# Performance work log

Measured on AMD Instinct MI355X. Metric: run time of the kernel, lower is better.

## Reference

```python
import jax, jax.numpy as jnp
import numpy as np


def _conv1x1(x, w, b):
    # x: [B,C,H,W], w: [O,C], b: [O] -> [B,O,H,W]
    return jnp.einsum('bchw,oc->bohw', x, w) + b[None, :, None, None]


def setup_inputs() -> dict:
    key = jax.random.key(0)
    ks = jax.random.split(key, 5)
    B, C, H, W = 4, 256, 64, 64
    C2 = C // 2
    scale = 0.02  # keep attention logits in a sane range
    return {
        'x': jax.random.normal(ks[0], (B, C, H, W), dtype=jnp.float32),
        'w_theta': jax.random.normal(ks[1], (C2, C), dtype=jnp.float32) * scale,
        'b_theta': jnp.zeros((C2,), dtype=jnp.float32),
        'w_phi': jax.random.normal(ks[2], (C2, C), dtype=jnp.float32) * scale,
        'b_phi': jnp.zeros((C2,), dtype=jnp.float32),
        'w_g': jax.random.normal(ks[3], (C2, C), dtype=jnp.float32) * scale,
        'b_g': jnp.zeros((C2,), dtype=jnp.float32),
        'w_out': jax.random.normal(ks[4], (C, C2), dtype=jnp.float32) * scale,
        'b_out': jnp.zeros((C,), dtype=jnp.float32),
    }


def reference(x, w_theta, b_theta, w_phi, b_phi, w_g, b_g, w_out, b_out):
    B, C, H, W = x.shape
    C2 = C // 2
    N = H * W
    theta = _conv1x1(x, w_theta, b_theta).reshape(B, C2, N)  # [B,C2,N]
    phi = _conv1x1(x, w_phi, b_phi).reshape(B, C2, N)        # [B,C2,N]
    g = _conv1x1(x, w_g, b_g).reshape(B, C2, N)              # [B,C2,N]
    # non-local attention: scores[b,m,n] = theta[b,:,m] . phi[b,:,n]
    scores = jnp.einsum('bcm,bcn->bmn', theta, phi)          # [B,N,N]
    attn = jax.nn.softmax(scores, axis=-1)                   # [B,N,N]
    # output = g @ attn^T : out[b,c,m] = sum_n g[b,c,n] * attn[b,m,n]
    out = jnp.einsum('bcn,bmn->bcm', g, attn)                # [B,C2,N]
    out = out.reshape(B, C2, H, W)
    return x + _conv1x1(out, w_out, b_out)
```

## Files before the change

### kernel.cpp

```cpp
#include <hip/hip_runtime.h>
#include <hip/hip_bf16.h>

#define B_  4
#define C_  256
#define C2_ 128
#define N_  4096
#define LOG2E 1.4426950408889634f

typedef unsigned short u16;
typedef __attribute__((ext_vector_type(8))) short bf16x8;
typedef __attribute__((ext_vector_type(4))) float f32x4;

static __device__ __forceinline__ u16 f2bf(float f) {
    return __builtin_bit_cast(u16, __float2bfloat16(f));
}
static __device__ __forceinline__ float bf2f(u16 u) {
    return __bfloat162float(__builtin_bit_cast(__hip_bfloat16, u));
}

__global__ __launch_bounds__(256) void prepw_kernel(
    const float* __restrict__ wt, const float* __restrict__ wp,
    const float* __restrict__ wg, const float* __restrict__ wo,
    u16* __restrict__ Wb) {
    int i = (blockIdx.x * 256 + threadIdx.x) * 4;
    int mat = i >> 15, off = i & 32767;
    const float* src = mat == 0 ? wt : (mat == 1 ? wp : (mat == 2 ? wg : wo));
    float4 v = *(const float4*)(src + off);
    ushort4 o = { f2bf(v.x), f2bf(v.y), f2bf(v.z), f2bf(v.w) };
    *(ushort4*)(Wb + i) = o;
}

__global__ __launch_bounds__(256) void projx_kernel(
    const float* __restrict__ x, const u16* __restrict__ Wb,
    const float* __restrict__ b_theta, const float* __restrict__ b_phi,
    const float* __restrict__ b_g,
    u16* __restrict__ Q, u16* __restrict__ K, u16* __restrict__ V) {
    __shared__ __align__(16) union {
        u16 XTs[32][264];
        u16 Vt[128][40];
    } sm;
    int bid = blockIdx.x;
    int b   = bid / (N_ / 32);
    int n0  = (bid % (N_ / 32)) * 32;
    int tid = threadIdx.x;
    int wave = tid >> 6, lane = tid & 63, quad = lane >> 4, l16 = lane & 15;
    int mgrp = wave >> 1, chalf = wave & 1;

#pragma unroll
    for (int it = 0; it < 4; ++it) {
        int idx = it * 256 + tid;
        int q = idx & 7, p = idx >> 3;
        const float* r0 = x + ((size_t)b * C_ + 2 * p) * N_ + n0 + 4 * q;
        float4 v0 = *(const float4*)r0;
        float4 v1 = *(const float4*)(r0 + N_);
        const float* f0 = (const float*)&v0;
        const float* f1 = (const float*)&v1;
#pragma unroll
        for (int j = 0; j < 4; ++j) {
            unsigned pk = (unsigned)f2bf(f0[j]) | ((unsigned)f2bf(f1[j]) << 16);
            *(unsigned*)&sm.XTs[4 * q + j][2 * p] = pk;
        }
    }
    __syncthreads();

    bf16x8 af[8];
#pragma unroll
    for (int ks = 0; ks < 8; ++ks)
        af[ks] = *(const bf16x8*)&sm.XTs[mgrp * 16 + l16][ks * 32 + quad * 8];
    __syncthreads();

    const float* biases[3] = { b_theta, b_phi, b_g };
#pragma unroll
    for (int mat = 0; mat < 3; ++mat) {
        const u16* wm = Wb + (size_t)mat * C2_ * C_;
        const float* bias = biases[mat];
        f32x4 acc[4];
#pragma unroll
        for (int i = 0; i < 4; ++i) acc[i] = (f32x4){0.f, 0.f, 0.f, 0.f};
#pragma unroll
        for (int ct = 0; ct < 4; ++ct) {
            int ce = chalf * 4 + ct;
            const u16* wr = wm + (size_t)(ce * 16 + l16) * C_ + quad * 8;
#pragma unroll
            for (int ks = 0; ks < 8; ++ks) {
                bf16x8 bf = *(const bf16x8*)(wr + ks * 32);
                acc[ct] = __builtin_amdgcn_mfma_f32_16x16x32_bf16(af[ks], bf, acc[ct], 0, 0, 0);
            }
        }
        if (mat < 2) {
            u16* dst = mat == 0 ? Q : K;
            float sc = mat == 0 ? LOG2E : 1.0f;
#pragma unroll
            for (int ct = 0; ct < 4; ++ct) {
                int c2 = (chalf * 4 + ct) * 16 + l16;
                float bb = bias[c2];
#pragma unroll
                for (int r = 0; r < 4; ++r) {
                    int n = n0 + mgrp * 16 + quad * 4 + r;
                    dst[((size_t)b * N_ + n) * C2_ + c2] = f2bf((acc[ct][r] + bb) * sc);
                }
            }
        } else {
#pragma unroll
            for (int ct = 0; ct < 4; ++ct) {
                int c2 = (chalf * 4 + ct) * 16 + l16;
                float bb = bias[c2];
#pragma unroll
                for (int r = 0; r < 4; ++r)
                    sm.Vt[c2][mgrp * 16 + quad * 4 + r] = f2bf(acc[ct][r] + bb);
            }
        }
    }
    __syncthreads();
    {
        int row = tid >> 1, col16 = (tid & 1) * 16;
        uint4 a0 = *(const uint4*)&sm.Vt[row][col16];
        uint4 a1 = *(const uint4*)&sm.Vt[row][col16 + 8];
        u16* vp = V + ((size_t)b * C2_ + row) * N_ + n0 + col16;
        *(uint4*)vp = a0;
        *(uint4*)(vp + 8) = a1;
    }
}

__global__ __launch_bounds__(256, 2) void attn_kernel(
    const u16* __restrict__ Q, const u16* __restrict__ K,
    const u16* __restrict__ V, u16* __restrict__ AO,
    u16* __restrict__ Opb, float* __restrict__ lsum, int nsplit) {
    const int BM = 128, BN = 64, D = C2_;
    const int per = B_ * (N_ / BM);
    int s    = blockIdx.x / per;
    int r0   = blockIdx.x % per;
    int b    = r0 / (N_ / BM);
    int m0   = (r0 % (N_ / BM)) * BM;
    int tid  = threadIdx.x;
    int wave = tid >> 6, lane = tid & 63, quad = (lane >> 4) & 3, l16 = lane & 15;

    __shared__ __align__(16) u16 Ks[BN][D + 8];
    __shared__ __align__(16) u16 Vs[D][BN + 8];
    __shared__ __align__(16) u16 Psb[4][32][BN + 8];
    u16* Ps = &Psb[wave][0][0];

    bf16x8 qf[2][4];
#pragma unroll
    for (int ms = 0; ms < 2; ++ms) {
        const u16* qp = Q + ((size_t)b * N_ + m0 + wave * 32 + ms * 16 + l16) * D;
#pragma unroll
        for (int kk = 0; kk < 4; ++kk)
            qf[ms][kk] = *(const bf16x8*)(qp + kk * 32 + quad * 8);
    }

    float l_r[2][4] = {{0.f, 0.f, 0.f, 0.f}, {0.f, 0.f, 0.f, 0.f}};
    f32x4 o_acc[2][8];
#pragma unroll
    for (int ms = 0; ms < 2; ++ms)
#pragma unroll
        for (int i = 0; i < 8; ++i) o_acc[ms][i] = (f32x4){0.f, 0.f, 0.f, 0.f};

    const int tiles = N_ / BN;
    const int base = tiles / nsplit, rem = tiles % nsplit;
    const int t0 = s * base + (s < rem ? s : rem);
    const int cnt = base + (s < rem ? 1 : 0);
    const int nt0 = t0 * BN, nt1 = (t0 + cnt) * BN;

    for (int nt = nt0; nt < nt1; nt += BN) {
        const u16* kp = K + ((size_t)b * N_ + nt) * D;
#pragma unroll
        for (int it = 0; it < 4; ++it) {
            int idx = it * 256 + tid;
            int row = idx >> 4, col = (idx & 15) * 8;
            *(uint4*)&Ks[row][col] = *(const uint4*)(kp + row * D + col);
        }
#pragma unroll
        for (int it = 0; it < 4; ++it) {
            int idx = it * 256 + tid;
            int row = idx >> 3, col = (idx & 7) * 8;
            *(uint4*)&Vs[row][col] =
                *(const uint4*)(V + ((size_t)b * C2_ + row) * N_ + nt + col);
        }
        __syncthreads();

        f32x4 sc[2][4];
#pragma unroll
        for (int nn = 0; nn < 4; ++nn) {
            f32x4 a0 = (f32x4){0.f, 0.f, 0.f, 0.f};
            f32x4 a1 = (f32x4){0.f, 0.f, 0.f, 0.f};
#pragma unroll
            for (int kk = 0; kk < 4; ++kk) {
                bf16x8 kf = *(const bf16x8*)&Ks[nn * 16 + l16][kk * 32 + quad * 8];
                a0 = __builtin_amdgcn_mfma_f32_16x16x32_bf16(qf[0][kk], kf, a0, 0, 0, 0);
                a1 = __builtin_amdgcn_mfma_f32_16x16x32_bf16(qf[1][kk], kf, a1, 0, 0, 0);
            }
            sc[0][nn] = a0;
            sc[1][nn] = a1;
        }

#pragma unroll
        for (int ms = 0; ms < 2; ++ms)
#pragma unroll
            for (int nn = 0; nn < 4; ++nn)
#pragma unroll
                for (int r = 0; r < 4; ++r) {
                    float p = __builtin_amdgcn_exp2f(sc[ms][nn][r]);
                    l_r[ms][r] += p;
                    Ps[(ms * 16 + quad * 4 + r) * (BN + 8) + nn * 16 + l16] = f2bf(p);
                }

#pragma unroll
        for (int ks = 0; ks < 2; ++ks) {
            bf16x8 pf0 = *(const bf16x8*)&Ps[(l16) * (BN + 8) + ks * 32 + quad * 8];
            bf16x8 pf1 = *(const bf16x8*)&Ps[(16 + l16) * (BN + 8) + ks * 32 + quad * 8];
#pragma unroll
            for (int cs = 0; cs < 8; ++cs) {
                bf16x8 vf = *(const bf16x8*)&Vs[cs * 16 + l16][ks * 32 + quad * 8];
                o_acc[0][cs] = __builtin_amdgcn_mfma_f32_16x16x32_bf16(pf0, vf, o_acc[0][cs], 0, 0, 0);
                o_acc[1][cs] = __builtin_amdgcn_mfma_f32_16x16x32_bf16(pf1, vf, o_acc[1][cs], 0, 0, 0);
            }
        }
        __syncthreads();
    }

#pragma unroll
    for (int ms = 0; ms < 2; ++ms)
#pragma unroll
        for (int r = 0; r < 4; ++r) {
            l_r[ms][r] += __shfl_xor(l_r[ms][r], 1);
            l_r[ms][r] += __shfl_xor(l_r[ms][r], 2);
            l_r[ms][r] += __shfl_xor(l_r[ms][r], 4);
            l_r[ms][r] += __shfl_xor(l_r[ms][r], 8);
        }

    if (Opb) {
#pragma unroll
        for (int ms = 0; ms < 2; ++ms) {
#pragma unroll
            for (int cs = 0; cs < 8; ++cs)
#pragma unroll
                for (int r = 0; r < 4; ++r) {
                    size_t row = (size_t)s * (B_ * N_) + (size_t)b * N_ +
                                 m0 + wave * 32 + ms * 16 + quad * 4 + r;
                    Opb[row * C2_ + cs * 16 + l16] = f2bf(o_acc[ms][cs][r]);
                }
            if (l16 == 0)
#pragma unroll
                for (int r = 0; r < 4; ++r) {
                    size_t row = (size_t)s * (B_ * N_) + (size_t)b * N_ +
                                 m0 + wave * 32 + ms * 16 + quad * 4 + r;
                    lsum[row] = l_r[ms][r];
                }
        }
    } else {
#pragma unroll
        for (int ms = 0; ms < 2; ++ms)
#pragma unroll
            for (int cs = 0; cs < 8; ++cs)
#pragma unroll
                for (int r = 0; r < 4; ++r) {
                    float v = o_acc[ms][cs][r] / l_r[ms][r];
                    AO[((size_t)b * N_ + m0 + wave * 32 + ms * 16 + quad * 4 + r) * C2_ +
                       cs * 16 + l16] = f2bf(v);
                }
    }
}

__global__ __launch_bounds__(256) void outproj_kernel(
    const float* __restrict__ x, const u16* __restrict__ Opb,
    const float* __restrict__ lsum, const u16* __restrict__ AO,
    const u16* __restrict__ Wob, const float* __restrict__ b_out,
    float* __restrict__ y, int nsplit) {
    __shared__ __align__(16) u16 As[64][C2_ + 8];
    __shared__ float Ls[64];
    int bid = blockIdx.x;
    int per_b = (C_ / 64) * (N_ / 64);
    int b   = bid / per_b;
    int rem = bid % per_b;
    int c0  = (rem / (N_ / 64)) * 64;
    int n0  = (rem % (N_ / 64)) * 64;
    int tid = threadIdx.x;
    int wave = tid >> 6, lane = tid & 63, quad = lane >> 4, l16 = lane & 15;

    if (nsplit > 1) {
        if (tid < 64) {
            float L = 0.f;
            for (int s = 0; s < nsplit; ++s)
                L += lsum[(size_t)s * (B_ * N_) + (size_t)b * N_ + n0 + tid];
            Ls[tid] = 1.f / L;
        }
        __syncthreads();
#pragma unroll
        for (int it = 0; it < 4; ++it) {
            int idx = it * 256 + tid;
            int n = idx >> 4, c8 = (idx & 15) * 8;
            float a[8] = {0.f, 0.f, 0.f, 0.f, 0.f, 0.f, 0.f, 0.f};
            for (int s = 0; s < nsplit; ++s) {
                const u16* op = Opb +
                    ((size_t)s * (B_ * N_) + (size_t)b * N_ + n0 + n) * C2_ + c8;
                uint4 raw = *(const uint4*)op;
                const u16* rp = (const u16*)&raw;
#pragma unroll
                for (int j = 0; j < 8; ++j) a[j] += bf2f(rp[j]);
            }
            float inv = Ls[n];
            u16 o[8];
#pragma unroll
            for (int j = 0; j < 8; ++j) o[j] = f2bf(a[j] * inv);
            *(uint4*)&As[n][c8] = *(const uint4*)o;
        }
    } else {
#pragma unroll
        for (int it = 0; it < 4; ++it) {
            int idx = it * 256 + tid;
            int n = idx >> 4, c8 = (idx & 15) * 8;
            *(uint4*)&As[n][c8] =
                *(const uint4*)(AO + ((size_t)b * N_ + n0 + n) * C2_ + c8);
        }
    }
    __syncthreads();

    int cw = c0 + wave * 16;
    bf16x8 af[4];
#pragma unroll
    for (int kk = 0; kk < 4; ++kk)
        af[kk] = *(const bf16x8*)&Wob[(size_t)(cw + l16) * C2_ + kk * 32 + quad * 8];

    f32x4 acc[4];
#pragma unroll
    for (int i = 0; i < 4; ++i) acc[i] = (f32x4){0.f, 0.f, 0.f, 0.f};

#pragma unroll
    for (int nn = 0; nn < 4; ++nn)
#pragma unroll
        for (int kk = 0; kk < 4; ++kk) {
            bf16x8 bf = *(const bf16x8*)&As[nn * 16 + l16][kk * 32 + quad * 8];
            acc[nn] = __builtin_amdgcn_mfma_f32_16x16x32_bf16(af[kk], bf, acc[nn], 0, 0, 0);
        }

    float bo[4];
#pragma unroll
    for (int r = 0; r < 4; ++r) bo[r] = b_out[cw + quad * 4 + r];

#pragma unroll
    for (int nn = 0; nn < 4; ++nn)
#pragma unroll
        for (int r = 0; r < 4; ++r) {
            int c = cw + quad * 4 + r;
            size_t off = ((size_t)b * C_ + c) * N_ + n0 + nn * 16 + l16;
            y[off] = x[off] + bo[r] + acc[nn][r];
        }
}

extern "C" void kernel_launch(void* const* d_in, const int* in_sizes, int n_in,
                              void* d_out, int out_size, void* d_ws, size_t ws_size,
                              hipStream_t stream) {
    const float* x       = (const float*)d_in[0];
    const float* w_theta = (const float*)d_in[1];
    const float* b_theta = (const float*)d_in[2];
    const float* w_phi   = (const float*)d_in[3];
    const float* b_phi   = (const float*)d_in[4];
    const float* w_g     = (const float*)d_in[5];
    const float* b_g     = (const float*)d_in[6];
    const float* w_out   = (const float*)d_in[7];
    const float* b_out   = (const float*)d_in[8];
    float* y = (float*)d_out;

    const size_t SZ = (size_t)B_ * N_ * C2_;
    u16* Q  = (u16*)d_ws;
    u16* K  = Q + SZ;
    u16* V  = K + SZ;
    u16* AO = V + SZ;
    u16* Wb = AO + SZ;
    u16* Wob = Wb + (size_t)3 * C2_ * C_;
    char* dyn = (char*)(Wb + (size_t)4 * C2_ * C_);
    size_t fixedB = (size_t)(dyn - (char*)d_ws);

    size_t perS = SZ * 2 + (size_t)B_ * N_ * 4;

    int S;
    if      (ws_size >= fixedB + 6 * perS) S = 6;
    else if (ws_size >= fixedB + 4 * perS) S = 4;
    else if (ws_size >= fixedB + 2 * perS) S = 2;
    else                                   S = 1;

    u16*   Opb = nullptr;
    float* ls  = nullptr;
    if (S > 1) {
        Opb = (u16*)dyn;
        ls  = (float*)(Opb + (size_t)S * SZ);
    }

    prepw_kernel<<<128, 256, 0, stream>>>(w_theta, w_phi, w_g, w_out, Wb);
    projx_kernel<<<B_ * (N_ / 32), 256, 0, stream>>>(
        x, Wb, b_theta, b_phi, b_g, Q, K, V);
    attn_kernel<<<B_ * (N_ / 128) * S, 256, 0, stream>>>(Q, K, V, AO, Opb, ls, S);
    outproj_kernel<<<B_ * (C_ / 64) * (N_ / 64), 256, 0, stream>>>(
        x, Opb, ls, AO, Wob, b_out, y, S);
}
```

Measured before the change: 179.8 us.

## Double attention row tile, drop weight prep kernel, allow eight-way split

Each attention wave now processes 64 query rows instead of 32, so every K/V tile loaded into shared memory is reused across twice as many rows. The separate weight-to-bf16 kernel is removed; projection kernels read fp32 weights and convert them inline. The key split count can rise to 8 to keep enough blocks. The larger per-wave accumulators raise register pressure, which risks spills or lower occupancy.

```diff
diff --git a/kernel.cpp b/kernel.cpp
--- a/kernel.cpp
+++ b/kernel.cpp
@@ -17,21 +17,17 @@
 static __device__ __forceinline__ float bf2f(u16 u) {
     return __bfloat162float(__builtin_bit_cast(__hip_bfloat16, u));
 }
-
-__global__ __launch_bounds__(256) void prepw_kernel(
+static __device__ __forceinline__ bf16x8 cvt8(const float* p) {
+    u16 t[8];
+#pragma unroll
+    for (int j = 0; j < 8; ++j) t[j] = f2bf(p[j]);
+    return *(const bf16x8*)t;
+}
+
+__global__ __launch_bounds__(256) void projx_kernel(
+    const float* __restrict__ x,
     const float* __restrict__ wt, const float* __restrict__ wp,
-    const float* __restrict__ wg, const float* __restrict__ wo,
-    u16* __restrict__ Wb) {
-    int i = (blockIdx.x * 256 + threadIdx.x) * 4;
-    int mat = i >> 15, off = i & 32767;
-    const float* src = mat == 0 ? wt : (mat == 1 ? wp : (mat == 2 ? wg : wo));
-    float4 v = *(const float4*)(src + off);
-    ushort4 o = { f2bf(v.x), f2bf(v.y), f2bf(v.z), f2bf(v.w) };
-    *(ushort4*)(Wb + i) = o;
-}
-
-__global__ __launch_bounds__(256) void projx_kernel(
-    const float* __restrict__ x, const u16* __restrict__ Wb,
+    const float* __restrict__ wg,
     const float* __restrict__ b_theta, const float* __restrict__ b_phi,
     const float* __restrict__ b_g,
     u16* __restrict__ Q, u16* __restrict__ K, u16* __restrict__ V) {
@@ -69,10 +65,11 @@
         af[ks] = *(const bf16x8*)&sm.XTs[mgrp * 16 + l16][ks * 32 + quad * 8];
     __syncthreads();
 
+    const float* wms[3]    = { wt, wp, wg };
     const float* biases[3] = { b_theta, b_phi, b_g };
 #pragma unroll
     for (int mat = 0; mat < 3; ++mat) {
-        const u16* wm = Wb + (size_t)mat * C2_ * C_;
+        const float* wm = wms[mat];
         const float* bias = biases[mat];
         f32x4 acc[4];
 #pragma unroll
@@ -80,10 +77,13 @@
 #pragma unroll
         for (int ct = 0; ct < 4; ++ct) {
             int ce = chalf * 4 + ct;
-            const u16* wr = wm + (size_t)(ce * 16 + l16) * C_ + quad * 8;
+            const float* wr = wm + (size_t)(ce * 16 + l16) * C_ + quad * 8;
 #pragma unroll
             for (int ks = 0; ks < 8; ++ks) {
-                bf16x8 bf = *(const bf16x8*)(wr + ks * 32);
+                float w8[8];
+                *(float4*)&w8[0] = *(const float4*)(wr + ks * 32);
+                *(float4*)&w8[4] = *(const float4*)(wr + ks * 32 + 4);
+                bf16x8 bf = cvt8(w8);
                 acc[ct] = __builtin_amdgcn_mfma_f32_16x16x32_bf16(af[ks], bf, acc[ct], 0, 0, 0);
             }
         }
@@ -126,7 +126,7 @@
     const u16* __restrict__ Q, const u16* __restrict__ K,
     const u16* __restrict__ V, u16* __restrict__ AO,
     u16* __restrict__ Opb, float* __restrict__ lsum, int nsplit) {
-    const int BM = 128, BN = 64, D = C2_;
+    const int BM = 256, BN = 64, D = C2_;
     const int per = B_ * (N_ / BM);
     int s    = blockIdx.x / per;
     int r0   = blockIdx.x % per;
@@ -137,22 +137,26 @@
 
     __shared__ __align__(16) u16 Ks[BN][D + 8];
     __shared__ __align__(16) u16 Vs[D][BN + 8];
-    __shared__ __align__(16) u16 Psb[4][32][BN + 8];
+    __shared__ __align__(16) u16 Psb[4][64][BN + 8];
     u16* Ps = &Psb[wave][0][0];
 
-    bf16x8 qf[2][4];
-#pragma unroll
-    for (int ms = 0; ms < 2; ++ms) {
-        const u16* qp = Q + ((size_t)b * N_ + m0 + wave * 32 + ms * 16 + l16) * D;
+    bf16x8 qf[4][4];
+#pragma unroll
+    for (int ms = 0; ms < 4; ++ms) {
+        const u16* qp = Q + ((size_t)b * N_ + m0 + wave * 64 + ms * 16 + l16) * D;
 #pragma unroll
         for (int kk = 0; kk < 4; ++kk)
             qf[ms][kk] = *(const bf16x8*)(qp + kk * 32 + quad * 8);
     }
 
-    float l_r[2][4] = {{0.f, 0.f, 0.f, 0.f}, {0.f, 0.f, 0.f, 0.f}};
-    f32x4 o_acc[2][8];
-#pragma unroll
-    for (int ms = 0; ms < 2; ++ms)
+    float l_r[4][4];
+#pragma unroll
+    for (int ms = 0; ms < 4; ++ms)
+#pragma unroll
+        for (int r = 0; r < 4; ++r) l_r[ms][r] = 0.f;
+    f32x4 o_acc[4][8];
+#pragma unroll
+    for (int ms = 0; ms < 4; ++ms)
 #pragma unroll
         for (int i = 0; i < 8; ++i) o_acc[ms][i] = (f32x4){0.f, 0.f, 0.f, 0.f};
 
@@ -179,48 +183,47 @@
         }
         __syncthreads();
 
-        f32x4 sc[2][4];
 #pragma unroll
         for (int nn = 0; nn < 4; ++nn) {
-            f32x4 a0 = (f32x4){0.f, 0.f, 0.f, 0.f};
-            f32x4 a1 = (f32x4){0.f, 0.f, 0.f, 0.f};
+            f32x4 a[4];
+#pragma unroll
+            for (int ms = 0; ms < 4; ++ms) a[ms] = (f32x4){0.f, 0.f, 0.f, 0.f};
 #pragma unroll
             for (int kk = 0; kk < 4; ++kk) {
                 bf16x8 kf = *(const bf16x8*)&Ks[nn * 16 + l16][kk * 32 + quad * 8];
-                a0 = __builtin_amdgcn_mfma_f32_16x16x32_bf16(qf[0][kk], kf, a0, 0, 0, 0);
-                a1 = __builtin_amdgcn_mfma_f32_16x16x32_bf16(qf[1][kk], kf, a1, 0, 0, 0);
-            }
-            sc[0][nn] = a0;
-            sc[1][nn] = a1;
-        }
-
-#pragma unroll
-        for (int ms = 0; ms < 2; ++ms)
-#pragma unroll
-            for (int nn = 0; nn < 4; ++nn)
+#pragma unroll
+                for (int ms = 0; ms < 4; ++ms)
+                    a[ms] = __builtin_amdgcn_mfma_f32_16x16x32_bf16(qf[ms][kk], kf, a[ms], 0, 0, 0);
+            }
+#pragma unroll
+            for (int ms = 0; ms < 4; ++ms)
 #pragma unroll
                 for (int r = 0; r < 4; ++r) {
-                    float p = __builtin_amdgcn_exp2f(sc[ms][nn][r]);
+                    float p = __builtin_amdgcn_exp2f(a[ms][r]);
                     l_r[ms][r] += p;
                     Ps[(ms * 16 + quad * 4 + r) * (BN + 8) + nn * 16 + l16] = f2bf(p);
                 }
+        }
 
 #pragma unroll
         for (int ks = 0; ks < 2; ++ks) {
-            bf16x8 pf0 = *(const bf16x8*)&Ps[(l16) * (BN + 8) + ks * 32 + quad * 8];
-            bf16x8 pf1 = *(const bf16x8*)&Ps[(16 + l16) * (BN + 8) + ks * 32 + quad * 8];
+            bf16x8 pf[4];
+#pragma unroll
+            for (int ms = 0; ms < 4; ++ms)
+                pf[ms] = *(const bf16x8*)&Ps[(ms * 16 + l16) * (BN + 8) + ks * 32 + quad * 8];
 #pragma unroll
             for (int cs = 0; cs < 8; ++cs) {
                 bf16x8 vf = *(const bf16x8*)&Vs[cs * 16 + l16][ks * 32 + quad * 8];
-                o_acc[0][cs] = __builtin_amdgcn_mfma_f32_16x16x32_bf16(pf0, vf, o_acc[0][cs], 0, 0, 0);
-                o_acc[1][cs] = __builtin_amdgcn_mfma_f32_16x16x32_bf16(pf1, vf, o_acc[1][cs], 0, 0, 0);
+#pragma unroll
+                for (int ms = 0; ms < 4; ++ms)
+                    o_acc[ms][cs] = __builtin_amdgcn_mfma_f32_16x16x32_bf16(pf[ms], vf, o_acc[ms][cs], 0, 0, 0);
             }
         }
         __syncthreads();
     }
 
 #pragma unroll
-    for (int ms = 0; ms < 2; ++ms)
+    for (int ms = 0; ms < 4; ++ms)
 #pragma unroll
         for (int r = 0; r < 4; ++r) {
             l_r[ms][r] += __shfl_xor(l_r[ms][r], 1);
@@ -231,32 +234,32 @@
 
     if (Opb) {
 #pragma unroll
-        for (int ms = 0; ms < 2; ++ms) {
+        for (int ms = 0; ms < 4; ++ms) {
 #pragma unroll
             for (int cs = 0; cs < 8; ++cs)
 #pragma unroll
                 for (int r = 0; r < 4; ++r) {
                     size_t row = (size_t)s * (B_ * N_) + (size_t)b * N_ +
-                                 m0 + wave * 32 + ms * 16 + quad * 4 + r;
+                                 m0 + wave * 64 + ms * 16 + quad * 4 + r;
                     Opb[row * C2_ + cs * 16 + l16] = f2bf(o_acc[ms][cs][r]);
                 }
             if (l16 == 0)
 #pragma unroll
                 for (int r = 0; r < 4; ++r) {
                     size_t row = (size_t)s * (B_ * N_) + (size_t)b * N_ +
-                                 m0 + wave * 32 + ms * 16 + quad * 4 + r;
+                                 m0 + wave * 64 + ms * 16 + quad * 4 + r;
                     lsum[row] = l_r[ms][r];
                 }
         }
     } else {
 #pragma unroll
-        for (int ms = 0; ms < 2; ++ms)
+        for (int ms = 0; ms < 4; ++ms)
 #pragma unroll
             for (int cs = 0; cs < 8; ++cs)
 #pragma unroll
                 for (int r = 0; r < 4; ++r) {
                     float v = o_acc[ms][cs][r] / l_r[ms][r];
-                    AO[((size_t)b * N_ + m0 + wave * 32 + ms * 16 + quad * 4 + r) * C2_ +
+                    AO[((size_t)b * N_ + m0 + wave * 64 + ms * 16 + quad * 4 + r) * C2_ +
                        cs * 16 + l16] = f2bf(v);
                 }
     }
@@ -265,7 +268,7 @@
 __global__ __launch_bounds__(256) void outproj_kernel(
     const float* __restrict__ x, const u16* __restrict__ Opb,
     const float* __restrict__ lsum, const u16* __restrict__ AO,
-    const u16* __restrict__ Wob, const float* __restrict__ b_out,
+    const float* __restrict__ w_out, const float* __restrict__ b_out,
     float* __restrict__ y, int nsplit) {
     __shared__ __align__(16) u16 As[64][C2_ + 8];
     __shared__ float Ls[64];
@@ -318,9 +321,16 @@
 
     int cw = c0 + wave * 16;
     bf16x8 af[4];
-#pragma unroll
-    for (int kk = 0; kk < 4; ++kk)
-        af[kk] = *(const bf16x8*)&Wob[(size_t)(cw + l16) * C2_ + kk * 32 + quad * 8];
+    {
+        const float* wrow = w_out + (size_t)(cw + l16) * C2_ + quad * 8;
+#pragma unroll
+        for (int kk = 0; kk < 4; ++kk) {
+            float w8[8];
+            *(float4*)&w8[0] = *(const float4*)(wrow + kk * 32);
+            *(float4*)&w8[4] = *(const float4*)(wrow + kk * 32 + 4);
+            af[kk] = cvt8(w8);
+        }
+    }
 
     f32x4 acc[4];
 #pragma unroll
@@ -366,20 +376,19 @@
     u16* Q  = (u16*)d_ws;
     u16* K  = Q + SZ;
     u16* V  = K + SZ;
-    u16* AO = V + SZ;
-    u16* Wb = AO + SZ;
-    u16* Wob = Wb + (size_t)3 * C2_ * C_;
-    char* dyn = (char*)(Wb + (size_t)4 * C2_ * C_);
+    char* dyn = (char*)(V + SZ);
     size_t fixedB = (size_t)(dyn - (char*)d_ws);
 
     size_t perS = SZ * 2 + (size_t)B_ * N_ * 4;
 
     int S;
-    if      (ws_size >= fixedB + 6 * perS) S = 6;
+    if      (ws_size >= fixedB + 8 * perS) S = 8;
+    else if (ws_size >= fixedB + 6 * perS) S = 6;
     else if (ws_size >= fixedB + 4 * perS) S = 4;
     else if (ws_size >= fixedB + 2 * perS) S = 2;
     else                                   S = 1;
 
+    u16*   AO  = (u16*)dyn;
     u16*   Opb = nullptr;
     float* ls  = nullptr;
     if (S > 1) {
@@ -387,10 +396,9 @@
         ls  = (float*)(Opb + (size_t)S * SZ);
     }
 
-    prepw_kernel<<<128, 256, 0, stream>>>(w_theta, w_phi, w_g, w_out, Wb);
     projx_kernel<<<B_ * (N_ / 32), 256, 0, stream>>>(
-        x, Wb, b_theta, b_phi, b_g, Q, K, V);
-    attn_kernel<<<B_ * (N_ / 128) * S, 256, 0, stream>>>(Q, K, V, AO, Opb, ls, S);
+        x, w_theta, w_phi, w_g, b_theta, b_phi, b_g, Q, K, V);
+    attn_kernel<<<B_ * (N_ / 256) * S, 256, 0, stream>>>(Q, K, V, AO, Opb, ls, S);
     outproj_kernel<<<B_ * (C_ / 64) * (N_ / 64), 256, 0, stream>>>(
-        x, Opb, ls, AO, Wob, b_out, y, S);
-}
+        x, Opb, ls, AO, w_out, b_out, y, S);
+}
```

After: 254.2 us. +41.4%, slower.

## Fuse projection, attention and output projection into one persistent kernel with grid barriers

Applied to the files above, without the earlier changes.

Replaces the four separate launches (weight prep, QKV projection, attention, output projection) with a single persistent kernel that runs each phase as a grid-stride loop and separates phases with atomic-counter grid barriers. Weights are converted from fp32 to bf16 inline instead of in a prep kernel, and the KV split count is capped at 4 so the grid is 128*S blocks. The aim is to remove launch gaps and the weight-prep pass, at the cost of spin-wait barriers that rely on all blocks being co-resident, plus an added memset per call.

```diff
diff --git a/kernel.cpp b/kernel.cpp
--- a/kernel.cpp
+++ b/kernel.cpp
@@ -17,335 +17,360 @@
 static __device__ __forceinline__ float bf2f(u16 u) {
     return __bfloat162float(__builtin_bit_cast(__hip_bfloat16, u));
 }
-
-__global__ __launch_bounds__(256) void prepw_kernel(
+static __device__ __forceinline__ bf16x8 cvt8(const float* p) {
+    u16 t[8];
+#pragma unroll
+    for (int j = 0; j < 8; ++j) t[j] = f2bf(p[j]);
+    return *(const bf16x8*)t;
+}
+
+static __device__ __forceinline__ void grid_barrier(unsigned* cnt, unsigned target) {
+    __syncthreads();
+    if (threadIdx.x == 0) {
+        __threadfence();
+        __hip_atomic_fetch_add(cnt, 1u, __ATOMIC_ACQ_REL, __HIP_MEMORY_SCOPE_AGENT);
+        while (__hip_atomic_load(cnt, __ATOMIC_ACQUIRE, __HIP_MEMORY_SCOPE_AGENT) < target) {
+            __builtin_amdgcn_s_sleep(8);
+        }
+    }
+    __syncthreads();
+}
+
+__global__ __launch_bounds__(256, 2) void fused_kernel(
+    const float* __restrict__ x,
     const float* __restrict__ wt, const float* __restrict__ wp,
-    const float* __restrict__ wg, const float* __restrict__ wo,
-    u16* __restrict__ Wb) {
-    int i = (blockIdx.x * 256 + threadIdx.x) * 4;
-    int mat = i >> 15, off = i & 32767;
-    const float* src = mat == 0 ? wt : (mat == 1 ? wp : (mat == 2 ? wg : wo));
-    float4 v = *(const float4*)(src + off);
-    ushort4 o = { f2bf(v.x), f2bf(v.y), f2bf(v.z), f2bf(v.w) };
-    *(ushort4*)(Wb + i) = o;
-}
-
-__global__ __launch_bounds__(256) void projx_kernel(
-    const float* __restrict__ x, const u16* __restrict__ Wb,
+    const float* __restrict__ wg,
     const float* __restrict__ b_theta, const float* __restrict__ b_phi,
     const float* __restrict__ b_g,
-    u16* __restrict__ Q, u16* __restrict__ K, u16* __restrict__ V) {
-    __shared__ __align__(16) union {
-        u16 XTs[32][264];
-        u16 Vt[128][40];
-    } sm;
-    int bid = blockIdx.x;
-    int b   = bid / (N_ / 32);
-    int n0  = (bid % (N_ / 32)) * 32;
-    int tid = threadIdx.x;
-    int wave = tid >> 6, lane = tid & 63, quad = lane >> 4, l16 = lane & 15;
-    int mgrp = wave >> 1, chalf = wave & 1;
-
-#pragma unroll
-    for (int it = 0; it < 4; ++it) {
-        int idx = it * 256 + tid;
-        int q = idx & 7, p = idx >> 3;
-        const float* r0 = x + ((size_t)b * C_ + 2 * p) * N_ + n0 + 4 * q;
-        float4 v0 = *(const float4*)r0;
-        float4 v1 = *(const float4*)(r0 + N_);
-        const float* f0 = (const float*)&v0;
-        const float* f1 = (const float*)&v1;
-#pragma unroll
-        for (int j = 0; j < 4; ++j) {
-            unsigned pk = (unsigned)f2bf(f0[j]) | ((unsigned)f2bf(f1[j]) << 16);
-            *(unsigned*)&sm.XTs[4 * q + j][2 * p] = pk;
-        }
-    }
-    __syncthreads();
-
-    bf16x8 af[8];
-#pragma unroll
-    for (int ks = 0; ks < 8; ++ks)
-        af[ks] = *(const bf16x8*)&sm.XTs[mgrp * 16 + l16][ks * 32 + quad * 8];
-    __syncthreads();
-
-    const float* biases[3] = { b_theta, b_phi, b_g };
-#pragma unroll
-    for (int mat = 0; mat < 3; ++mat) {
-        const u16* wm = Wb + (size_t)mat * C2_ * C_;
-        const float* bias = biases[mat];
-        f32x4 acc[4];
-#pragma unroll
-        for (int i = 0; i < 4; ++i) acc[i] = (f32x4){0.f, 0.f, 0.f, 0.f};
-#pragma unroll
-        for (int ct = 0; ct < 4; ++ct) {
-            int ce = chalf * 4 + ct;
-            const u16* wr = wm + (size_t)(ce * 16 + l16) * C_ + quad * 8;
-#pragma unroll
-            for (int ks = 0; ks < 8; ++ks) {
-                bf16x8 bf = *(const bf16x8*)(wr + ks * 32);
-                acc[ct] = __builtin_amdgcn_mfma_f32_16x16x32_bf16(af[ks], bf, acc[ct], 0, 0, 0);
-            }
-        }
-        if (mat < 2) {
-            u16* dst = mat == 0 ? Q : K;
-            float sc = mat == 0 ? LOG2E : 1.0f;
-#pragma unroll
-            for (int ct = 0; ct < 4; ++ct) {
-                int c2 = (chalf * 4 + ct) * 16 + l16;
-                float bb = bias[c2];
-#pragma unroll
-                for (int r = 0; r < 4; ++r) {
-                    int n = n0 + mgrp * 16 + quad * 4 + r;
-                    dst[((size_t)b * N_ + n) * C2_ + c2] = f2bf((acc[ct][r] + bb) * sc);
-                }
-            }
-        } else {
-#pragma unroll
-            for (int ct = 0; ct < 4; ++ct) {
-                int c2 = (chalf * 4 + ct) * 16 + l16;
-                float bb = bias[c2];
-#pragma unroll
-                for (int r = 0; r < 4; ++r)
-                    sm.Vt[c2][mgrp * 16 + quad * 4 + r] = f2bf(acc[ct][r] + bb);
-            }
-        }
-    }
-    __syncthreads();
-    {
-        int row = tid >> 1, col16 = (tid & 1) * 16;
-        uint4 a0 = *(const uint4*)&sm.Vt[row][col16];
-        uint4 a1 = *(const uint4*)&sm.Vt[row][col16 + 8];
-        u16* vp = V + ((size_t)b * C2_ + row) * N_ + n0 + col16;
-        *(uint4*)vp = a0;
-        *(uint4*)(vp + 8) = a1;
-    }
-}
-
-__global__ __launch_bounds__(256, 2) void attn_kernel(
-    const u16* __restrict__ Q, const u16* __restrict__ K,
-    const u16* __restrict__ V, u16* __restrict__ AO,
-    u16* __restrict__ Opb, float* __restrict__ lsum, int nsplit) {
-    const int BM = 128, BN = 64, D = C2_;
-    const int per = B_ * (N_ / BM);
-    int s    = blockIdx.x / per;
-    int r0   = blockIdx.x % per;
-    int b    = r0 / (N_ / BM);
-    int m0   = (r0 % (N_ / BM)) * BM;
+    const float* __restrict__ w_out, const float* __restrict__ b_out,
+    float* __restrict__ y,
+    u16* __restrict__ Q, u16* __restrict__ K, u16* __restrict__ V,
+    u16* __restrict__ AO, u16* __restrict__ Opb, float* __restrict__ lsum,
+    unsigned* __restrict__ bar, int nsplit) {
+    __shared__ __align__(16) u16 smA[64][136];
+    __shared__ __align__(16) u16 smB[128][72];
+    __shared__ __align__(16) u16 smC[4][32][72];
+
     int tid  = threadIdx.x;
     int wave = tid >> 6, lane = tid & 63, quad = (lane >> 4) & 3, l16 = lane & 15;
-
-    __shared__ __align__(16) u16 Ks[BN][D + 8];
-    __shared__ __align__(16) u16 Vs[D][BN + 8];
-    __shared__ __align__(16) u16 Psb[4][32][BN + 8];
-    u16* Ps = &Psb[wave][0][0];
-
-    bf16x8 qf[2][4];
-#pragma unroll
-    for (int ms = 0; ms < 2; ++ms) {
-        const u16* qp = Q + ((size_t)b * N_ + m0 + wave * 32 + ms * 16 + l16) * D;
-#pragma unroll
-        for (int kk = 0; kk < 4; ++kk)
-            qf[ms][kk] = *(const bf16x8*)(qp + kk * 32 + quad * 8);
+    const unsigned target = gridDim.x;
+
+    {
+        u16* XTs = (u16*)smA;
+        u16 (*Vt)[40] = (u16(*)[40])smB;
+        int mgrp = wave >> 1, chalf = wave & 1;
+        const float* wms[3]    = { wt, wp, wg };
+        const float* biases[3] = { b_theta, b_phi, b_g };
+
+        for (int wb = blockIdx.x; wb < B_ * (N_ / 32); wb += gridDim.x) {
+            int b  = wb / (N_ / 32);
+            int n0 = (wb % (N_ / 32)) * 32;
+
+#pragma unroll
+            for (int it = 0; it < 4; ++it) {
+                int idx = it * 256 + tid;
+                int q = idx & 7, p = idx >> 3;
+                const float* r0 = x + ((size_t)b * C_ + 2 * p) * N_ + n0 + 4 * q;
+                float4 v0 = *(const float4*)r0;
+                float4 v1 = *(const float4*)(r0 + N_);
+                const float* f0 = (const float*)&v0;
+                const float* f1 = (const float*)&v1;
+#pragma unroll
+                for (int j = 0; j < 4; ++j) {
+                    unsigned pk = (unsigned)f2bf(f0[j]) | ((unsigned)f2bf(f1[j]) << 16);
+                    *(unsigned*)&XTs[(size_t)(4 * q + j) * 264 + 2 * p] = pk;
+                }
+            }
+            __syncthreads();
+
+            bf16x8 af[8];
+#pragma unroll
+            for (int ks = 0; ks < 8; ++ks)
+                af[ks] = *(const bf16x8*)
+                    &XTs[(size_t)(mgrp * 16 + l16) * 264 + ks * 32 + quad * 8];
+            __syncthreads();
+
+#pragma unroll
+            for (int mat = 0; mat < 3; ++mat) {
+                const float* wm = wms[mat];
+                const float* bias = biases[mat];
+                f32x4 acc[4];
+#pragma unroll
+                for (int i = 0; i < 4; ++i) acc[i] = (f32x4){0.f, 0.f, 0.f, 0.f};
+#pragma unroll
+                for (int ct = 0; ct < 4; ++ct) {
+                    int ce = chalf * 4 + ct;
+                    const float* wr = wm + (size_t)(ce * 16 + l16) * C_ + quad * 8;
+#pragma unroll
+                    for (int ks = 0; ks < 8; ++ks) {
+                        float w8[8];
+                        *(float4*)&w8[0] = *(const float4*)(wr + ks * 32);
+                        *(float4*)&w8[4] = *(const float4*)(wr + ks * 32 + 4);
+                        bf16x8 bf = cvt8(w8);
+                        acc[ct] = __builtin_amdgcn_mfma_f32_16x16x32_bf16(
+                            af[ks], bf, acc[ct], 0, 0, 0);
+                    }
+                }
+                if (mat < 2) {
+                    u16* dst = mat == 0 ? Q : K;
+                    float sc = mat == 0 ? LOG2E : 1.0f;
+#pragma unroll
+                    for (int ct = 0; ct < 4; ++ct) {
+                        int c2 = (chalf * 4 + ct) * 16 + l16;
+                        float bb = bias[c2];
+#pragma unroll
+                        for (int r = 0; r < 4; ++r) {
+                            int n = n0 + mgrp * 16 + quad * 4 + r;
+                            dst[((size_t)b * N_ + n) * C2_ + c2] =
+                                f2bf((acc[ct][r] + bb) * sc);
+                        }
+                    }
+                } else {
+#pragma unroll
+                    for (int ct = 0; ct < 4; ++ct) {
+                        int c2 = (chalf * 4 + ct) * 16 + l16;
+                        float bb = bias[c2];
+#pragma unroll
+                        for (int r = 0; r < 4; ++r)
+                            Vt[c2][mgrp * 16 + quad * 4 + r] = f2bf(acc[ct][r] + bb);
+                    }
+                }
+            }
+            __syncthreads();
+            {
+                int row = tid >> 1, col16 = (tid & 1) * 16;
+                uint4 a0 = *(const uint4*)&Vt[row][col16];
+                uint4 a1 = *(const uint4*)&Vt[row][col16 + 8];
+                u16* vp = V + ((size_t)b * C2_ + row) * N_ + n0 + col16;
+                *(uint4*)vp = a0;
+                *(uint4*)(vp + 8) = a1;
+            }
+            __syncthreads();
+        }
     }
-
-    float l_r[2][4] = {{0.f, 0.f, 0.f, 0.f}, {0.f, 0.f, 0.f, 0.f}};
-    f32x4 o_acc[2][8];
-#pragma unroll
-    for (int ms = 0; ms < 2; ++ms)
-#pragma unroll
-        for (int i = 0; i < 8; ++i) o_acc[ms][i] = (f32x4){0.f, 0.f, 0.f, 0.f};
-
-    const int tiles = N_ / BN;
-    const int base = tiles / nsplit, rem = tiles % nsplit;
-    const int t0 = s * base + (s < rem ? s : rem);
-    const int cnt = base + (s < rem ? 1 : 0);
-    const int nt0 = t0 * BN, nt1 = (t0 + cnt) * BN;
-
-    for (int nt = nt0; nt < nt1; nt += BN) {
-        const u16* kp = K + ((size_t)b * N_ + nt) * D;
-#pragma unroll
-        for (int it = 0; it < 4; ++it) {
-            int idx = it * 256 + tid;
-            int row = idx >> 4, col = (idx & 15) * 8;
-            *(uint4*)&Ks[row][col] = *(const uint4*)(kp + row * D + col);
-        }
-#pragma unroll
-        for (int it = 0; it < 4; ++it) {
-            int idx = it * 256 + tid;
-            int row = idx >> 3, col = (idx & 7) * 8;
-            *(uint4*)&Vs[row][col] =
-                *(const uint4*)(V + ((size_t)b * C2_ + row) * N_ + nt + col);
-        }
-        __syncthreads();
-
-        f32x4 sc[2][4];
-#pragma unroll
-        for (int nn = 0; nn < 4; ++nn) {
-            f32x4 a0 = (f32x4){0.f, 0.f, 0.f, 0.f};
-            f32x4 a1 = (f32x4){0.f, 0.f, 0.f, 0.f};
-#pragma unroll
-            for (int kk = 0; kk < 4; ++kk) {
-                bf16x8 kf = *(const bf16x8*)&Ks[nn * 16 + l16][kk * 32 + quad * 8];
-                a0 = __builtin_amdgcn_mfma_f32_16x16x32_bf16(qf[0][kk], kf, a0, 0, 0, 0);
-                a1 = __builtin_amdgcn_mfma_f32_16x16x32_bf16(qf[1][kk], kf, a1, 0, 0, 0);
-            }
-            sc[0][nn] = a0;
-            sc[1][nn] = a1;
-        }
-
+    grid_barrier(&bar[0], target);
+
+    {
+        const int BM = 128, BN = 64, D = C2_;
+        const int per = B_ * (N_ / BM);
+        int s  = blockIdx.x / per;
+        int r0 = blockIdx.x % per;
+        int b  = r0 / (N_ / BM);
+        int m0 = (r0 % (N_ / BM)) * BM;
+
+        u16 (*Ks)[136] = (u16(*)[136])smA;
+        u16 (*Vs)[72]  = (u16(*)[72])smB;
+        u16* Ps = &smC[wave][0][0];
+
+        bf16x8 qf[2][4];
+#pragma unroll
+        for (int ms = 0; ms < 2; ++ms) {
+            const u16* qp = Q + ((size_t)b * N_ + m0 + wave * 32 + ms * 16 + l16) * D;
+#pragma unroll
+            for (int kk = 0; kk < 4; ++kk)
+                qf[ms][kk] = *(const bf16x8*)(qp + kk * 32 + quad * 8);
+        }
+
+        float l_r[2][4] = {{0.f, 0.f, 0.f, 0.f}, {0.f, 0.f, 0.f, 0.f}};
+        f32x4 o_acc[2][8];
 #pragma unroll
         for (int ms = 0; ms < 2; ++ms)
 #pragma unroll
+            for (int i = 0; i < 8; ++i) o_acc[ms][i] = (f32x4){0.f, 0.f, 0.f, 0.f};
+
+        const int chunk = N_ / nsplit;
+        const int nt0 = s * chunk, nt1 = nt0 + chunk;
+
+        for (int nt = nt0; nt < nt1; nt += BN) {
+            const u16* kp = K + ((size_t)b * N_ + nt) * D;
+#pragma unroll
+            for (int it = 0; it < 4; ++it) {
+                int idx = it * 256 + tid;
+                int row = idx >> 4, col = (idx & 15) * 8;
+                *(uint4*)&Ks[row][col] = *(const uint4*)(kp + row * D + col);
+            }
+#pragma unroll
+            for (int it = 0; it < 4; ++it) {
+                int idx = it * 256 + tid;
+                int row = idx >> 3, col = (idx & 7) * 8;
+                *(uint4*)&Vs[row][col] =
+                    *(const uint4*)(V + ((size_t)b * C2_ + row) * N_ + nt + col);
+            }
+            __syncthreads();
+
+            f32x4 sc[2][4];
+#pragma unroll
+            for (int nn = 0; nn < 4; ++nn) {
+                f32x4 a0 = (f32x4){0.f, 0.f, 0.f, 0.f};
+                f32x4 a1 = (f32x4){0.f, 0.f, 0.f, 0.f};
+#pragma unroll
+                for (int kk = 0; kk < 4; ++kk) {
+                    bf16x8 kf = *(const bf16x8*)&Ks[nn * 16 + l16][kk * 32 + quad * 8];
+                    a0 = __builtin_amdgcn_mfma_f32_16x16x32_bf16(qf[0][kk], kf, a0, 0, 0, 0);
+                    a1 = __builtin_amdgcn_mfma_f32_16x16x32_bf16(qf[1][kk], kf, a1, 0, 0, 0);
+                }
+                sc[0][nn] = a0;
+                sc[1][nn] = a1;
+            }
+
+#pragma unroll
+            for (int ms = 0; ms < 2; ++ms)
+#pragma unroll
+                for (int nn = 0; nn < 4; ++nn)
+#pragma unroll
+                    for (int r = 0; r < 4; ++r) {
+                        float p = __builtin_amdgcn_exp2f(sc[ms][nn][r]);
+                        l_r[ms][r] += p;
+                        Ps[(ms * 16 + quad * 4 + r) * 72 + nn * 16 + l16] = f2bf(p);
+                    }
+
+#pragma unroll
+            for (int ks = 0; ks < 2; ++ks) {
+                bf16x8 pf0 = *(const bf16x8*)&Ps[(l16) * 72 + ks * 32 + quad * 8];
+                bf16x8 pf1 = *(const bf16x8*)&Ps[(16 + l16) * 72 + ks * 32 + quad * 8];
+#pragma unroll
+                for (int cs = 0; cs < 8; ++cs) {
+                    bf16x8 vf = *(const bf16x8*)&Vs[cs * 16 + l16][ks * 32 + quad * 8];
+                    o_acc[0][cs] = __builtin_amdgcn_mfma_f32_16x16x32_bf16(pf0, vf, o_acc[0][cs], 0, 0, 0);
+                    o_acc[1][cs] = __builtin_amdgcn_mfma_f32_16x16x32_bf16(pf1, vf, o_acc[1][cs], 0, 0, 0);
+                }
+            }
+            __syncthreads();
+        }
+
+#pragma unroll
+        for (int ms = 0; ms < 2; ++ms)
+#pragma unroll
+            for (int r = 0; r < 4; ++r) {
+                l_r[ms][r] += __shfl_xor(l_r[ms][r], 1);
+                l_r[ms][r] += __shfl_xor(l_r[ms][r], 2);
+                l_r[ms][r] += __shfl_xor(l_r[ms][r], 4);
+                l_r[ms][r] += __shfl_xor(l_r[ms][r], 8);
+            }
+
+        if (nsplit > 1) {
+#pragma unroll
+            for (int ms = 0; ms < 2; ++ms) {
+#pragma unroll
+                for (int cs = 0; cs < 8; ++cs)
+#pragma unroll
+                    for (int r = 0; r < 4; ++r) {
+                        size_t row = (size_t)s * (B_ * N_) + (size_t)b * N_ +
+                                     m0 + wave * 32 + ms * 16 + quad * 4 + r;
+                        Opb[row * C2_ + cs * 16 + l16] = f2bf(o_acc[ms][cs][r]);
+                    }
+                if (l16 == 0)
+#pragma unroll
+                    for (int r = 0; r < 4; ++r) {
+                        size_t row = (size_t)s * (B_ * N_) + (size_t)b * N_ +
+                                     m0 + wave * 32 + ms * 16 + quad * 4 + r;
+                        lsum[row] = l_r[ms][r];
+                    }
+            }
+        } else {
+#pragma unroll
+            for (int ms = 0; ms < 2; ++ms)
+#pragma unroll
+                for (int cs = 0; cs < 8; ++cs)
+#pragma unroll
+                    for (int r = 0; r < 4; ++r) {
+                        float v = o_acc[ms][cs][r] / l_r[ms][r];
+                        AO[((size_t)b * N_ + m0 + wave * 32 + ms * 16 + quad * 4 + r) * C2_ +
+                           cs * 16 + l16] = f2bf(v);
+                    }
+        }
+    }
+    grid_barrier(&bar[1], target);
+
+    {
+        u16 (*As)[136] = (u16(*)[136])smA;
+        float* Ls = (float*)smC;
+        const int per_b = (C_ / 64) * (N_ / 64);
+        const int tiles = B_ * per_b;
+
+        for (int t = blockIdx.x; t < tiles; t += gridDim.x) {
+            int b   = t / per_b;
+            int rem = t % per_b;
+            int c0  = (rem / (N_ / 64)) * 64;
+            int n0  = (rem % (N_ / 64)) * 64;
+
+            if (nsplit > 1) {
+                if (tid < 64) {
+                    float L = 0.f;
+                    for (int s = 0; s < nsplit; ++s)
+                        L += lsum[(size_t)s * (B_ * N_) + (size_t)b * N_ + n0 + tid];
+                    Ls[tid] = 1.f / L;
+                }
+                __syncthreads();
+#pragma unroll
+                for (int it = 0; it < 4; ++it) {
+                    int idx = it * 256 + tid;
+                    int n = idx >> 4, c8 = (idx & 15) * 8;
+                    float a[8] = {0.f, 0.f, 0.f, 0.f, 0.f, 0.f, 0.f, 0.f};
+                    for (int s = 0; s < nsplit; ++s) {
+                        const u16* op = Opb +
+                            ((size_t)s * (B_ * N_) + (size_t)b * N_ + n0 + n) * C2_ + c8;
+                        uint4 raw = *(const uint4*)op;
+                        const u16* rp = (const u16*)&raw;
+#pragma unroll
+                        for (int j = 0; j < 8; ++j) a[j] += bf2f(rp[j]);
+                    }
+                    float inv = Ls[n];
+                    u16 o[8];
+#pragma unroll
+                    for (int j = 0; j < 8; ++j) o[j] = f2bf(a[j] * inv);
+                    *(uint4*)&As[n][c8] = *(const uint4*)o;
+                }
+            } else {
+#pragma unroll
+                for (int it = 0; it < 4; ++it) {
+                    int idx = it * 256 + tid;
+                    int n = idx >> 4, c8 = (idx & 15) * 8;
+                    *(uint4*)&As[n][c8] =
+                        *(const uint4*)(AO + ((size_t)b * N_ + n0 + n) * C2_ + c8);
+                }
+            }
+            __syncthreads();
+
+            int cw = c0 + wave * 16;
+            bf16x8 af[4];
+            {
+                const float* wrow = w_out + (size_t)(cw + l16) * C2_ + quad * 8;
+#pragma unroll
+                for (int kk = 0; kk < 4; ++kk) {
+                    float w8[8];
+                    *(float4*)&w8[0] = *(const float4*)(wrow + kk * 32);
+                    *(float4*)&w8[4] = *(const float4*)(wrow + kk * 32 + 4);
+                    af[kk] = cvt8(w8);
+                }
+            }
+
+            f32x4 acc[4];
+#pragma unroll
+            for (int i = 0; i < 4; ++i) acc[i] = (f32x4){0.f, 0.f, 0.f, 0.f};
+#pragma unroll
             for (int nn = 0; nn < 4; ++nn)
 #pragma unroll
+                for (int kk = 0; kk < 4; ++kk) {
+                    bf16x8 bf = *(const bf16x8*)&As[nn * 16 + l16][kk * 32 + quad * 8];
+                    acc[nn] = __builtin_amdgcn_mfma_f32_16x16x32_bf16(af[kk], bf, acc[nn], 0, 0, 0);
+                }
+
+            float bo[4];
+#pragma unroll
+            for (int r = 0; r < 4; ++r) bo[r] = b_out[cw + quad * 4 + r];
+
+#pragma unroll
+            for (int nn = 0; nn < 4; ++nn)
+#pragma unroll
                 for (int r = 0; r < 4; ++r) {
-                    float p = __builtin_amdgcn_exp2f(sc[ms][nn][r]);
-                    l_r[ms][r] += p;
-                    Ps[(ms * 16 + quad * 4 + r) * (BN + 8) + nn * 16 + l16] = f2bf(p);
-                }
-
-#pragma unroll
-        for (int ks = 0; ks < 2; ++ks) {
-            bf16x8 pf0 = *(const bf16x8*)&Ps[(l16) * (BN + 8) + ks * 32 + quad * 8];
-            bf16x8 pf1 = *(const bf16x8*)&Ps[(16 + l16) * (BN + 8) + ks * 32 + quad * 8];
-#pragma unroll
-            for (int cs = 0; cs < 8; ++cs) {
-                bf16x8 vf = *(const bf16x8*)&Vs[cs * 16 + l16][ks * 32 + quad * 8];
-                o_acc[0][cs] = __builtin_amdgcn_mfma_f32_16x16x32_bf16(pf0, vf, o_acc[0][cs], 0, 0, 0);
-                o_acc[1][cs] = __builtin_amdgcn_mfma_f32_16x16x32_bf16(pf1, vf, o_acc[1][cs], 0, 0, 0);
-            }
-        }
-        __syncthreads();
+                    int c = cw + quad * 4 + r;
+                    size_t off = ((size_t)b * C_ + c) * N_ + n0 + nn * 16 + l16;
+                    y[off] = x[off] + bo[r] + acc[nn][r];
+                }
+            __syncthreads();
+        }
     }
-
-#pragma unroll
-    for (int ms = 0; ms < 2; ++ms)
-#pragma unroll
-        for (int r = 0; r < 4; ++r) {
-            l_r[ms][r] += __shfl_xor(l_r[ms][r], 1);
-            l_r[ms][r] += __shfl_xor(l_r[ms][r], 2);
-            l_r[ms][r] += __shfl_xor(l_r[ms][r], 4);
-            l_r[ms][r] += __shfl_xor(l_r[ms][r], 8);
-        }
-
-    if (Opb) {
-#pragma unroll
-        for (int ms = 0; ms < 2; ++ms) {
-#pragma unroll
-            for (int cs = 0; cs < 8; ++cs)
-#pragma unroll
-                for (int r = 0; r < 4; ++r) {
-                    size_t row = (size_t)s * (B_ * N_) + (size_t)b * N_ +
-                                 m0 + wave * 32 + ms * 16 + quad * 4 + r;
-                    Opb[row * C2_ + cs * 16 + l16] = f2bf(o_acc[ms][cs][r]);
-                }
-            if (l16 == 0)
-#pragma unroll
-                for (int r = 0; r < 4; ++r) {
-                    size_t row = (size_t)s * (B_ * N_) + (size_t)b * N_ +
-                                 m0 + wave * 32 + ms * 16 + quad * 4 + r;
-                    lsum[row] = l_r[ms][r];
-                }
-        }
-    } else {
-#pragma unroll
-        for (int ms = 0; ms < 2; ++ms)
-#pragma unroll
-            for (int cs = 0; cs < 8; ++cs)
-#pragma unroll
-                for (int r = 0; r < 4; ++r) {
-                    float v = o_acc[ms][cs][r] / l_r[ms][r];
-                    AO[((size_t)b * N_ + m0 + wave * 32 + ms * 16 + quad * 4 + r) * C2_ +
-                       cs * 16 + l16] = f2bf(v);
-                }
-    }
-}
-
-__global__ __launch_bounds__(256) void outproj_kernel(
-    const float* __restrict__ x, const u16* __restrict__ Opb,
-    const float* __restrict__ lsum, const u16* __restrict__ AO,
-    const u16* __restrict__ Wob, const float* __restrict__ b_out,
-    float* __restrict__ y, int nsplit) {
-    __shared__ __align__(16) u16 As[64][C2_ + 8];
-    __shared__ float Ls[64];
-    int bid = blockIdx.x;
-    int per_b = (C_ / 64) * (N_ / 64);
-    int b   = bid / per_b;
-    int rem = bid % per_b;
-    int c0  = (rem / (N_ / 64)) * 64;
-    int n0  = (rem % (N_ / 64)) * 64;
-    int tid = threadIdx.x;
-    int wave = tid >> 6, lane = tid & 63, quad = lane >> 4, l16 = lane & 15;
-
-    if (nsplit > 1) {
-        if (tid < 64) {
-            float L = 0.f;
-            for (int s = 0; s < nsplit; ++s)
-                L += lsum[(size_t)s * (B_ * N_) + (size_t)b * N_ + n0 + tid];
-            Ls[tid] = 1.f / L;
-        }
-        __syncthreads();
-#pragma unroll
-        for (int it = 0; it < 4; ++it) {
-            int idx = it * 256 + tid;
-            int n = idx >> 4, c8 = (idx & 15) * 8;
-            float a[8] = {0.f, 0.f, 0.f, 0.f, 0.f, 0.f, 0.f, 0.f};
-            for (int s = 0; s < nsplit; ++s) {
-                const u16* op = Opb +
-                    ((size_t)s * (B_ * N_) + (size_t)b * N_ + n0 + n) * C2_ + c8;
-                uint4 raw = *(const uint4*)op;
-                const u16* rp = (const u16*)&raw;
-#pragma unroll
-                for (int j = 0; j < 8; ++j) a[j] += bf2f(rp[j]);
-            }
-            float inv = Ls[n];
-            u16 o[8];
-#pragma unroll
-            for (int j = 0; j < 8; ++j) o[j] = f2bf(a[j] * inv);
-            *(uint4*)&As[n][c8] = *(const uint4*)o;
-        }
-    } else {
-#pragma unroll
-        for (int it = 0; it < 4; ++it) {
-            int idx = it * 256 + tid;
-            int n = idx >> 4, c8 = (idx & 15) * 8;
-            *(uint4*)&As[n][c8] =
-                *(const uint4*)(AO + ((size_t)b * N_ + n0 + n) * C2_ + c8);
-        }
-    }
-    __syncthreads();
-
-    int cw = c0 + wave * 16;
-    bf16x8 af[4];
-#pragma unroll
-    for (int kk = 0; kk < 4; ++kk)
-        af[kk] = *(const bf16x8*)&Wob[(size_t)(cw + l16) * C2_ + kk * 32 + quad * 8];
-
-    f32x4 acc[4];
-#pragma unroll
-    for (int i = 0; i < 4; ++i) acc[i] = (f32x4){0.f, 0.f, 0.f, 0.f};
-
-#pragma unroll
-    for (int nn = 0; nn < 4; ++nn)
-#pragma unroll
-        for (int kk = 0; kk < 4; ++kk) {
-            bf16x8 bf = *(const bf16x8*)&As[nn * 16 + l16][kk * 32 + quad * 8];
-            acc[nn] = __builtin_amdgcn_mfma_f32_16x16x32_bf16(af[kk], bf, acc[nn], 0, 0, 0);
-        }
-
-    float bo[4];
-#pragma unroll
-    for (int r = 0; r < 4; ++r) bo[r] = b_out[cw + quad * 4 + r];
-
-#pragma unroll
-    for (int nn = 0; nn < 4; ++nn)
-#pragma unroll
-        for (int r = 0; r < 4; ++r) {
-            int c = cw + quad * 4 + r;
-            size_t off = ((size_t)b * C_ + c) * N_ + n0 + nn * 16 + l16;
-            y[off] = x[off] + bo[r] + acc[nn][r];
-        }
 }
 
 extern "C" void kernel_launch(void* const* d_in, const int* in_sizes, int n_in,
@@ -363,34 +388,26 @@
     float* y = (float*)d_out;
 
     const size_t SZ = (size_t)B_ * N_ * C2_;
-    u16* Q  = (u16*)d_ws;
-    u16* K  = Q + SZ;
-    u16* V  = K + SZ;
-    u16* AO = V + SZ;
-    u16* Wb = AO + SZ;
-    u16* Wob = Wb + (size_t)3 * C2_ * C_;
-    char* dyn = (char*)(Wb + (size_t)4 * C2_ * C_);
+    u16* Q = (u16*)d_ws;
+    u16* K = Q + SZ;
+    u16* V = K + SZ;
+    unsigned* bar = (unsigned*)(V + SZ);
+    char* dyn = (char*)bar + 256;
     size_t fixedB = (size_t)(dyn - (char*)d_ws);
 
     size_t perS = SZ * 2 + (size_t)B_ * N_ * 4;
 
     int S;
-    if      (ws_size >= fixedB + 6 * perS) S = 6;
-    else if (ws_size >= fixedB + 4 * perS) S = 4;
+    if      (ws_size >= fixedB + 4 * perS) S = 4;
     else if (ws_size >= fixedB + 2 * perS) S = 2;
     else                                   S = 1;
 
-    u16*   Opb = nullptr;
-    float* ls  = nullptr;
-    if (S > 1) {
-        Opb = (u16*)dyn;
-        ls  = (float*)(Opb + (size_t)S * SZ);
-    }
-
-    prepw_kernel<<<128, 256, 0, stream>>>(w_theta, w_phi, w_g, w_out, Wb);
-    projx_kernel<<<B_ * (N_ / 32), 256, 0, stream>>>(
-        x, Wb, b_theta, b_phi, b_g, Q, K, V);
-    attn_kernel<<<B_ * (N_ / 128) * S, 256, 0, stream>>>(Q, K, V, AO, Opb, ls, S);
-    outproj_kernel<<<B_ * (C_ / 64) * (N_ / 64), 256, 0, stream>>>(
-        x, Opb, ls, AO, Wob, b_out, y, S);
-}
+    u16*   AO  = (u16*)dyn;
+    u16*   Opb = (u16*)dyn;
+    float* ls  = (float*)(Opb + (size_t)S * SZ);
+
+    hipMemsetAsync(bar, 0, 256, stream);
+    fused_kernel<<<dim3(128 * S), dim3(256), 0, stream>>>(
+        x, w_theta, w_phi, w_g, b_theta, b_phi, b_g, w_out, b_out, y,
+        Q, K, V, AO, Opb, ls, bar, S);
+}
```

Result: slower. 406.4 us (+126.1%).
